# Optimization experiments

Hardware: AMD Instinct MI355X
Metric: run time of the kernel (lower is better)

Reference implementation:

```python
import jax, jax.numpy as jnp
import numpy as np

K = 5      # kernel_size
STRIDE = 1
EPS = 1e-7


def _extract_patches(x, k, s):
    # x: [B,H,W,C] -> [B,Ho,Wo,k,k,C], same (kh,kw,c) layout as tf.extract_image_patches VALID
    B, H, W, C = x.shape
    Ho = (H - k) // s + 1
    Wo = (W - k) // s + 1
    r = (jnp.arange(Ho) * s)[:, None] + jnp.arange(k)   # [Ho,k]
    c = (jnp.arange(Wo) * s)[:, None] + jnp.arange(k)   # [Wo,k]
    return x[:, r[:, None, :, None], c[None, :, None, :], :]


def _rotate(pflat, angle, k):
    # Replicates tf.contrib.image.transform with angles_to_projective_transforms,
    # including the (1+1e-7) normalization of the 3x3 matrix in the original code.
    # pflat: [N, k*k, C], angle: [N]; bilinear sampling, fill value 0 outside.
    N = pflat.shape[0]
    f32 = pflat.dtype
    co, si = jnp.cos(angle), jnp.sin(angle)
    km1 = jnp.asarray(k - 1, f32)
    xoff = (km1 - (co * km1 - si * km1)) * 0.5
    yoff = (km1 - (si * km1 + co * km1)) * 0.5
    scale = 1.0 / (1.0 + EPS)  # transforms /= transforms[:, 8:9] + 1e-7
    gy, gx = jnp.meshgrid(jnp.arange(k, dtype=f32), jnp.arange(k, dtype=f32), indexing='ij')
    sx = (co[:, None, None] * gx - si[:, None, None] * gy + xoff[:, None, None]) * scale
    sy = (si[:, None, None] * gx + co[:, None, None] * gy + yoff[:, None, None]) * scale
    sx = sx.reshape(N, k * k)
    sy = sy.reshape(N, k * k)
    x0 = jnp.floor(sx)
    y0 = jnp.floor(sy)
    wx = (sx - x0)[..., None]
    wy = (sy - y0)[..., None]
    x0i = x0.astype(jnp.int32)
    y0i = y0.astype(jnp.int32)

    def samp(yi, xi):
        valid = (xi >= 0) & (xi < k) & (yi >= 0) & (yi < k)
        idx = jnp.clip(yi, 0, k - 1) * k + jnp.clip(xi, 0, k - 1)   # [N,k*k]
        v = jnp.take_along_axis(pflat, idx[..., None], axis=1)      # [N,k*k,C]
        return jnp.where(valid[..., None], v, jnp.zeros((), f32))

    v00 = samp(y0i, x0i)
    v01 = samp(y0i, x0i + 1)
    v10 = samp(y0i + 1, x0i)
    v11 = samp(y0i + 1, x0i + 1)
    top = v00 * (1 - wx) + v01 * wx
    bot = v10 * (1 - wx) + v11 * wx
    return top * (1 - wy) + bot * wy   # [N,k*k,C]


def _forward(input_tensor, W, b):
    k, s = K, STRIDE
    B, H, Wd, C = input_tensor.shape
    patches = _extract_patches(input_tensor, k, s)      # [B,Ho,Wo,k,k,C]
    Ho, Wo = patches.shape[1], patches.shape[2]
    inten = patches.sum(-1)                             # [B,Ho,Wo,k,k] channel-sum intensity
    ridx = jnp.arange(k, dtype=patches.dtype)
    tot = inten.sum((-2, -1)) + EPS
    cr = (inten * ridx[:, None]).sum((-2, -1)) / tot    # centroid row
    cc = (inten * ridx[None, :]).sum((-2, -1)) / tot    # centroid col
    m = (k - 1) / 2.0                                   # meanCenter (same for row/col)
    angle = jnp.arctan2(cr - m, cc - m + EPS)           # [B,Ho,Wo]
    pflat = patches.reshape(B * Ho * Wo, k * k, C)
    rot = _rotate(pflat, angle.reshape(-1), k)          # [N,k*k,C]
    rot = rot.reshape(B, Ho * Wo, k * k * C)
    wflat = W.reshape(W.shape[0], -1)                   # [F, k*k*C]
    out = jnp.einsum('bpd,fd->bpf', rot, wflat)         # elementwise-mult-sum 'conv'
    return out.reshape(B, Ho, Wo, -1) + b


def setup_inputs():
    key = jax.random.key(0)
    k1, k2 = jax.random.split(key, 2)
    B, H, Wd, C, F = 4, 128, 128, 16, 32
    input_tensor = jax.random.uniform(k1, (B, H, Wd, C), dtype=jnp.float32)
    lim = float(np.sqrt(6.0 / (K * K * C + F)))  # glorot_uniform
    W = jax.random.uniform(k2, (F, K, K, C), minval=-lim, maxval=lim, dtype=jnp.float32)
    b = jnp.zeros((F,), jnp.float32)
    return {"input_tensor": input_tensor, "W": W, "b": b}


def reference(input_tensor, W, b):
    return _forward(input_tensor, W, b)
```

## Files before the change

kernel.cpp:

```cpp
#include <hip/hip_runtime.h>


#define KS     5
#define TILE   8
#define TW     (TILE + KS - 1)
#define CPAD   20
#define C_IN   16
#define F_OUT  32
#define H_IN   128
#define W_IN   128
#define HO     124
#define WO     124
#define NBATCH 4
#define EPSF   1e-7f
#define BLOCK  256
#define KW     400

#define ANG_OFF     12160
#define RED_STRIDE  34
#define RED_WAVE    (64 * RED_STRIDE)
#define SMEM_BYTES  34816

typedef __attribute__((ext_vector_type(8))) short  short8;
typedef __attribute__((ext_vector_type(4))) float  floatx4;

static __device__ __forceinline__ short f2bf(float f) {
    union { float f; unsigned u; } v; v.f = f;
    unsigned r = v.u + 0x7fffu + ((v.u >> 16) & 1u);
    return (short)(r >> 16);
}

static __device__ __forceinline__ short8 blend8(
    const float* __restrict__ s_in, int lxq, int lyq,
    float co, float si, float xo, float yo, int t, int ch0)
{
    const float scl = 1.0f / (1.0f + EPSF);
    int ky = t / KS, kx = t - KS * ky;
    float sx = (co * (float)kx - si * (float)ky + xo) * scl;
    float sy = (si * (float)kx + co * (float)ky + yo) * scl;
    float fx0 = floorf(sx), fy0 = floorf(sy);
    float wx = sx - fx0, wy = sy - fy0;
    int x0 = (int)fx0, y0 = (int)fy0;
    int x1 = x0 + 1, y1 = y0 + 1;
    float vx0 = (x0 >= 0 && x0 < KS) ? 1.f : 0.f;
    float vx1 = (x1 >= 0 && x1 < KS) ? 1.f : 0.f;
    float vy0 = (y0 >= 0 && y0 < KS) ? 1.f : 0.f;
    float vy1 = (y1 >= 0 && y1 < KS) ? 1.f : 0.f;
    float w00 = (1.f - wx) * (1.f - wy) * vx0 * vy0;
    float w01 = wx * (1.f - wy) * vx1 * vy0;
    float w10 = (1.f - wx) * wy * vx0 * vy1;
    float w11 = wx * wy * vx1 * vy1;
    int cx0 = min(max(x0, 0), KS - 1), cx1 = min(max(x1, 0), KS - 1);
    int cy0 = min(max(y0, 0), KS - 1), cy1 = min(max(y1, 0), KS - 1);
    const float* p00 = &s_in[((lyq + cy0) * TW + (lxq + cx0)) * CPAD + ch0];
    const float* p01 = &s_in[((lyq + cy0) * TW + (lxq + cx1)) * CPAD + ch0];
    const float* p10 = &s_in[((lyq + cy1) * TW + (lxq + cx0)) * CPAD + ch0];
    const float* p11 = &s_in[((lyq + cy1) * TW + (lxq + cx1)) * CPAD + ch0];
    float r[8];
    #pragma unroll
    for (int cv = 0; cv < 2; ++cv) {
        float4 a = *(const float4*)(p00 + 4 * cv);
        float4 b = *(const float4*)(p01 + 4 * cv);
        float4 c = *(const float4*)(p10 + 4 * cv);
        float4 d = *(const float4*)(p11 + 4 * cv);
        r[4*cv+0] = w00 * a.x + w01 * b.x + w10 * c.x + w11 * d.x;
        r[4*cv+1] = w00 * a.y + w01 * b.y + w10 * c.y + w11 * d.y;
        r[4*cv+2] = w00 * a.z + w01 * b.z + w10 * c.z + w11 * d.z;
        r[4*cv+3] = w00 * a.w + w01 * b.w + w10 * c.w + w11 * d.w;
    }
    return (short8){f2bf(r[0]), f2bf(r[1]), f2bf(r[2]), f2bf(r[3]),
                    f2bf(r[4]), f2bf(r[5]), f2bf(r[6]), f2bf(r[7])};
}

__global__ __launch_bounds__(BLOCK, 2) void rotconv_kernel(
    const float* __restrict__ in, const float* __restrict__ Wg,
    const float* __restrict__ bg, float* __restrict__ out)
{
    __shared__ __align__(16) char smem[SMEM_BYTES];
    float*  s_in   = (float*)smem;
    float*  s_int  = (float*)(smem + 11520);
    float4* s_ang4 = (float4*)(smem + ANG_OFF);
    float*  red    = (float*)smem;

    const int tid  = threadIdx.x;
    const int bx = blockIdx.x, by = blockIdx.y, bimg = blockIdx.z;
    const int ox = bx * TILE, oy = by * TILE;

    const float* inb = in + (size_t)bimg * (H_IN * W_IN * C_IN);
    for (int i = tid; i < TW * TW * (C_IN / 4); i += BLOCK) {
        int cv = i & 3;
        int pp = i >> 2;
        int x = pp % TW, y = pp / TW;
        int gy = oy + y, gx = ox + x;
        float4 v = make_float4(0.f, 0.f, 0.f, 0.f);
        if (gy < H_IN && gx < W_IN)
            v = *(const float4*)(inb + ((size_t)(gy * W_IN + gx) * C_IN) + 4 * cv);
        *(float4*)(&s_in[pp * CPAD + 4 * cv]) = v;
    }
    __syncthreads();

    for (int pp = tid; pp < TW * TW; pp += BLOCK) {
        const float* sp = &s_in[pp * CPAD];
        float s = 0.f;
        #pragma unroll
        for (int c = 0; c < C_IN; ++c) s += sp[c];
        s_int[(pp / TW) * (TW + 1) + (pp % TW)] = s;
    }
    __syncthreads();

    if (tid < 64) {
        const int alx = tid & 7, aly = tid >> 3;
        float tot = EPSF, cr = 0.f, cc = 0.f;
        #pragma unroll
        for (int dy = 0; dy < KS; ++dy)
            #pragma unroll
            for (int dx = 0; dx < KS; ++dx) {
                float v = s_int[(aly + dy) * (TW + 1) + (alx + dx)];
                tot += v; cr += v * (float)dy; cc += v * (float)dx;
            }
        cr /= tot; cc /= tot;
        float ang = atan2f(cr - 2.0f, cc - 2.0f + EPSF);
        float si, co;
        sincosf(ang, &si, &co);
        float xoff = (4.0f - (co * 4.0f - si * 4.0f)) * 0.5f;
        float yoff = (4.0f - (si * 4.0f + co * 4.0f)) * 0.5f;
        s_ang4[tid] = make_float4(co, si, xoff, yoff);
    }
    __syncthreads();

    const int p    = tid & 63;
    const int wv   = tid >> 6;
    const int col  = p & 15;
    const int quad = p >> 4;

    float4 angs[4];
    #pragma unroll
    for (int m = 0; m < 4; ++m) angs[m] = s_ang4[16 * m + col];

    floatx4 acc[4][2];
    #pragma unroll
    for (int m = 0; m < 4; ++m) {
        acc[m][0] = (floatx4){0.f, 0.f, 0.f, 0.f};
        acc[m][1] = acc[m][0];
    }

    const int nstep = (wv == 0) ? 4 : 3;
    const int lxq = col & 7, lyq0 = col >> 3;
    const int ch0 = (quad & 1) * 8;
    const short8 zero8 = {0,0,0,0,0,0,0,0};

    #pragma unroll
    for (int s = 0; s < 4; ++s) {
        if (s < nstep) {
            const int ta = wv + 8 * s;
            const int tb = ta + 4;
            const int tq = (quad < 2) ? ta : tb;

            short8 bf0 = zero8, bf1 = zero8;
            if (tq < KS * KS) {
                const float* wp0 = Wg + (size_t)col * KW + tq * 16 + ch0;
                float4 a = *(const float4*)(wp0);
                float4 b = *(const float4*)(wp0 + 4);
                bf0 = (short8){f2bf(a.x), f2bf(a.y), f2bf(a.z), f2bf(a.w),
                               f2bf(b.x), f2bf(b.y), f2bf(b.z), f2bf(b.w)};
                const float* wp1 = wp0 + (size_t)16 * KW;
                float4 c = *(const float4*)(wp1);
                float4 d = *(const float4*)(wp1 + 4);
                bf1 = (short8){f2bf(c.x), f2bf(c.y), f2bf(c.z), f2bf(c.w),
                               f2bf(d.x), f2bf(d.y), f2bf(d.z), f2bf(d.w)};
            }

            #pragma unroll
            for (int m = 0; m < 4; ++m) {
                short8 av = zero8;
                if (tq < KS * KS)
                    av = blend8(s_in, lxq, 2 * m + lyq0,
                                angs[m].x, angs[m].y, angs[m].z, angs[m].w,
                                tq, ch0);
                acc[m][0] = __builtin_amdgcn_mfma_f32_16x16x32_bf16(av, bf0, acc[m][0], 0, 0, 0);
                acc[m][1] = __builtin_amdgcn_mfma_f32_16x16x32_bf16(av, bf1, acc[m][1], 0, 0, 0);
            }
        }
    }

    __syncthreads();
    #pragma unroll
    for (int m = 0; m < 4; ++m)
        #pragma unroll
        for (int n = 0; n < 2; ++n)
            #pragma unroll
            for (int r = 0; r < 4; ++r) {
                int px = 16 * m + 4 * quad + r;
                red[wv * RED_WAVE + px * RED_STRIDE + n * 16 + col] = acc[m][n][r];
            }
    __syncthreads();

    const int rpx = tid >> 2;
    const int rf0 = (tid & 3) * 8;
    float sum[8];
    #pragma unroll
    for (int j = 0; j < 8; ++j) sum[j] = bg[rf0 + j];
    #pragma unroll
    for (int w = 0; w < 4; ++w) {
        const float* rp = red + w * RED_WAVE + rpx * RED_STRIDE + rf0;
        #pragma unroll
        for (int j = 0; j < 8; ++j) sum[j] += rp[j];
    }
    const int ho = oy + (rpx >> 3), wo = ox + (rpx & 7);
    if (ho < HO && wo < WO) {
        float* op = out + (((size_t)bimg * HO + ho) * WO + wo) * F_OUT + rf0;
        *(float4*)op       = make_float4(sum[0], sum[1], sum[2], sum[3]);
        *(float4*)(op + 4) = make_float4(sum[4], sum[5], sum[6], sum[7]);
    }
}

extern "C" void kernel_launch(void* const* d_in, const int* in_sizes, int n_in,
                              void* d_out, int out_size, void* d_ws, size_t ws_size,
                              hipStream_t stream) {
    const float* in = (const float*)d_in[0];
    const float* Wg = (const float*)d_in[1];
    const float* bg = (const float*)d_in[2];
    float* out      = (float*)d_out;
    dim3 grid((WO + TILE - 1) / TILE, (HO + TILE - 1) / TILE, NBATCH);
    rotconv_kernel<<<grid, dim3(BLOCK), 0, stream>>>(in, Wg, bg, out);
}
```

Before: 74.09 us.

## Enlarge tile to 16x16, stage bf16 weights in LDS, drop cross-wave reduction

Raises the output tile from 8x8 to 16x16 so each block computes 256 pixels, and each wave now owns 4 full output rows across all 25 kernel taps instead of splitting taps across waves. This removes the shared-memory reduction of partial accumulators and its two barriers, and cuts halo reloading per output. Weights are converted to bf16 once per block into LDS instead of being reloaded and converted from global memory per step. The bias is folded into the accumulator init. In exchange, LDS use nearly doubles to about 64KB, which may lower occupancy, and each wave now runs 13 serial MFMA steps.

Measured after the change: 80.63 us. +8.8%, slower.

```diff
diff --git a/kernel.cpp b/kernel.cpp
--- a/kernel.cpp
+++ b/kernel.cpp
@@ -2,7 +2,7 @@
 
 
 #define KS     5
-#define TILE   8
+#define TILE   16
 #define TW     (TILE + KS - 1)
 #define CPAD   20
 #define C_IN   16
@@ -15,13 +15,15 @@
 #define EPSF   1e-7f
 #define BLOCK  256
 #define KW     400
-
-#define ANG_OFF     12160
-#define RED_STRIDE  34
-#define RED_WAVE    (64 * RED_STRIDE)
-#define SMEM_BYTES  34816
+#define SWS    408
+
+#define SINT_OFF 32000
+#define ANG_OFF  33680
+#define SW_OFF   37776
+#define SMEM_BYTES 63888
 
 typedef __attribute__((ext_vector_type(8))) short  short8;
+typedef __attribute__((ext_vector_type(4))) short  short4v;
 typedef __attribute__((ext_vector_type(4))) float  floatx4;
 
 static __device__ __forceinline__ short f2bf(float f) {
@@ -78,9 +80,9 @@
 {
     __shared__ __align__(16) char smem[SMEM_BYTES];
     float*  s_in   = (float*)smem;
-    float*  s_int  = (float*)(smem + 11520);
+    float*  s_int  = (float*)(smem + SINT_OFF);
     float4* s_ang4 = (float4*)(smem + ANG_OFF);
-    float*  red    = (float*)smem;
+    short*  sW     = (short*)(smem + SW_OFF);
 
     const int tid  = threadIdx.x;
     const int bx = blockIdx.x, by = blockIdx.y, bimg = blockIdx.z;
@@ -97,19 +99,30 @@
             v = *(const float4*)(inb + ((size_t)(gy * W_IN + gx) * C_IN) + 4 * cv);
         *(float4*)(&s_in[pp * CPAD + 4 * cv]) = v;
     }
+
+    for (int i = tid; i < (F_OUT * KW) / 4; i += BLOCK) {
+        int f = i / 100;
+        int k = (i - f * 100) * 4;
+        float4 w = *(const float4*)(Wg + (size_t)f * KW + k);
+        short4v h = {f2bf(w.x), f2bf(w.y), f2bf(w.z), f2bf(w.w)};
+        *(short4v*)(&sW[f * SWS + k]) = h;
+    }
     __syncthreads();
 
     for (int pp = tid; pp < TW * TW; pp += BLOCK) {
         const float* sp = &s_in[pp * CPAD];
-        float s = 0.f;
-        #pragma unroll
-        for (int c = 0; c < C_IN; ++c) s += sp[c];
+        float4 a = *(const float4*)(sp);
+        float4 b = *(const float4*)(sp + 4);
+        float4 c = *(const float4*)(sp + 8);
+        float4 d = *(const float4*)(sp + 12);
+        float s = ((a.x + a.y) + (a.z + a.w)) + ((b.x + b.y) + (b.z + b.w))
+                + ((c.x + c.y) + (c.z + c.w)) + ((d.x + d.y) + (d.z + d.w));
         s_int[(pp / TW) * (TW + 1) + (pp % TW)] = s;
     }
     __syncthreads();
 
-    if (tid < 64) {
-        const int alx = tid & 7, aly = tid >> 3;
+    {
+        const int alx = tid & 15, aly = tid >> 4;
         float tot = EPSF, cr = 0.f, cc = 0.f;
         #pragma unroll
         for (int dy = 0; dy < KS; ++dy)
@@ -132,85 +145,59 @@
     const int wv   = tid >> 6;
     const int col  = p & 15;
     const int quad = p >> 4;
+    const int ch0  = (quad & 1) * 8;
 
     float4 angs[4];
     #pragma unroll
-    for (int m = 0; m < 4; ++m) angs[m] = s_ang4[16 * m + col];
+    for (int m = 0; m < 4; ++m) angs[m] = s_ang4[(4 * wv + m) * 16 + col];
 
     floatx4 acc[4][2];
+    {
+        float bv0 = bg[col], bv1 = bg[col + 16];
+        #pragma unroll
+        for (int m = 0; m < 4; ++m) {
+            acc[m][0] = (floatx4){bv0, bv0, bv0, bv0};
+            acc[m][1] = (floatx4){bv1, bv1, bv1, bv1};
+        }
+    }
+
+    const short8 zero8 = {0,0,0,0,0,0,0,0};
+
+    for (int c = 0; c < 13; ++c) {
+        const int tq = 2 * c + (quad >> 1);
+        const bool val = (tq < KS * KS);
+
+        short8 bf0 = zero8, bf1 = zero8;
+        if (val) {
+            bf0 = *(const short8*)(&sW[col * SWS + tq * 16 + ch0]);
+            bf1 = *(const short8*)(&sW[(col + 16) * SWS + tq * 16 + ch0]);
+        }
+        #pragma unroll
+        for (int m = 0; m < 4; ++m) {
+            short8 av = zero8;
+            if (val)
+                av = blend8(s_in, col, 4 * wv + m,
+                            angs[m].x, angs[m].y, angs[m].z, angs[m].w,
+                            tq, ch0);
+            acc[m][0] = __builtin_amdgcn_mfma_f32_16x16x32_bf16(av, bf0, acc[m][0], 0, 0, 0);
+            acc[m][1] = __builtin_amdgcn_mfma_f32_16x16x32_bf16(av, bf1, acc[m][1], 0, 0, 0);
+        }
+    }
+
     #pragma unroll
     for (int m = 0; m < 4; ++m) {
-        acc[m][0] = (floatx4){0.f, 0.f, 0.f, 0.f};
-        acc[m][1] = acc[m][0];
-    }
-
-    const int nstep = (wv == 0) ? 4 : 3;
-    const int lxq = col & 7, lyq0 = col >> 3;
-    const int ch0 = (quad & 1) * 8;
-    const short8 zero8 = {0,0,0,0,0,0,0,0};
-
-    #pragma unroll
-    for (int s = 0; s < 4; ++s) {
-        if (s < nstep) {
-            const int ta = wv + 8 * s;
-            const int tb = ta + 4;
-            const int tq = (quad < 2) ? ta : tb;
-
-            short8 bf0 = zero8, bf1 = zero8;
-            if (tq < KS * KS) {
-                const float* wp0 = Wg + (size_t)col * KW + tq * 16 + ch0;
-                float4 a = *(const float4*)(wp0);
-                float4 b = *(const float4*)(wp0 + 4);
-                bf0 = (short8){f2bf(a.x), f2bf(a.y), f2bf(a.z), f2bf(a.w),
-                               f2bf(b.x), f2bf(b.y), f2bf(b.z), f2bf(b.w)};
-                const float* wp1 = wp0 + (size_t)16 * KW;
-                float4 c = *(const float4*)(wp1);
-                float4 d = *(const float4*)(wp1 + 4);
-                bf1 = (short8){f2bf(c.x), f2bf(c.y), f2bf(c.z), f2bf(c.w),
-                               f2bf(d.x), f2bf(d.y), f2bf(d.z), f2bf(d.w)};
-            }
-
-            #pragma unroll
-            for (int m = 0; m < 4; ++m) {
-                short8 av = zero8;
-                if (tq < KS * KS)
-                    av = blend8(s_in, lxq, 2 * m + lyq0,
-                                angs[m].x, angs[m].y, angs[m].z, angs[m].w,
-                                tq, ch0);
-                acc[m][0] = __builtin_amdgcn_mfma_f32_16x16x32_bf16(av, bf0, acc[m][0], 0, 0, 0);
-                acc[m][1] = __builtin_amdgcn_mfma_f32_16x16x32_bf16(av, bf1, acc[m][1], 0, 0, 0);
-            }
-        }
-    }
-
-    __syncthreads();
-    #pragma unroll
-    for (int m = 0; m < 4; ++m)
-        #pragma unroll
-        for (int n = 0; n < 2; ++n)
+        const int ho = oy + 4 * wv + m;
+        if (ho < HO) {
             #pragma unroll
             for (int r = 0; r < 4; ++r) {
-                int px = 16 * m + 4 * quad + r;
-                red[wv * RED_WAVE + px * RED_STRIDE + n * 16 + col] = acc[m][n][r];
+                const int wo = ox + 4 * quad + r;
+                if (wo < WO) {
+                    float* op = out + (((size_t)bimg * HO + ho) * WO + wo) * F_OUT + col;
+                    op[0]  = acc[m][0][r];
+                    op[16] = acc[m][1][r];
+                }
             }
-    __syncthreads();
-
-    const int rpx = tid >> 2;
-    const int rf0 = (tid & 3) * 8;
-    float sum[8];
-    #pragma unroll
-    for (int j = 0; j < 8; ++j) sum[j] = bg[rf0 + j];
-    #pragma unroll
-    for (int w = 0; w < 4; ++w) {
-        const float* rp = red + w * RED_WAVE + rpx * RED_STRIDE + rf0;
-        #pragma unroll
-        for (int j = 0; j < 8; ++j) sum[j] += rp[j];
-    }
-    const int ho = oy + (rpx >> 3), wo = ox + (rpx & 7);
-    if (ho < HO && wo < WO) {
-        float* op = out + (((size_t)bimg * HO + ho) * WO + wo) * F_OUT + rf0;
-        *(float4*)op       = make_float4(sum[0], sum[1], sum[2], sum[3]);
-        *(float4*)(op + 4) = make_float4(sum[4], sum[5], sum[6], sum[7]);
+        }
     }
 }
 
```
